# Kernel tuning notes

Measured on AMD Instinct MI355X. Metric: run time of the kernel, lower is better.

Reference implementation:

```python
import jax, jax.numpy as jnp
import numpy as np

HIDDEN = 768

def setup_inputs() -> dict:
    key = jax.random.key(0)
    ks = jax.random.split(key, 7)
    x = jax.random.normal(ks[0], (4, 4096, HIDDEN), dtype=jnp.float32)
    s = 1.0 / np.sqrt(HIDDEN)
    Wq = jax.random.uniform(ks[1], (HIDDEN, HIDDEN), minval=-s, maxval=s, dtype=jnp.float32)
    Wk = jax.random.uniform(ks[2], (HIDDEN, HIDDEN), minval=-s, maxval=s, dtype=jnp.float32)
    Wv = jax.random.uniform(ks[3], (HIDDEN, HIDDEN), minval=-s, maxval=s, dtype=jnp.float32)
    bq = jax.random.uniform(ks[4], (HIDDEN,), minval=-s, maxval=s, dtype=jnp.float32)
    bk = jax.random.uniform(ks[5], (HIDDEN,), minval=-s, maxval=s, dtype=jnp.float32)
    bv = jax.random.uniform(ks[6], (HIDDEN,), minval=-s, maxval=s, dtype=jnp.float32)
    return {"x": x, "Wq": Wq, "bq": bq, "Wk": Wk, "bk": bk, "Wv": Wv, "bv": bv}

def reference(x, Wq, bq, Wk, bk, Wv, bv):
    # q,k,v: [b, s, d]
    q = jnp.einsum('bsd,de->bse', x, Wq.T) + bq
    k = jnp.einsum('bsd,de->bse', x, Wk.T) + bk
    v = jnp.einsum('bsd,de->bse', x, Wv.T) + bv
    scale = 1.0 / jnp.sqrt(jnp.asarray(x.shape[-1], dtype=x.dtype))
    scores = jnp.einsum('bqd,bkd->bqk', q, k) * scale  # [b, s, s]
    attn = jax.nn.softmax(scores, axis=-1)
    return jnp.einsum('bqk,bkd->bqd', attn, v)
```

## Files before the change

kernel.cpp:

```cpp
#include <hip/hip_runtime.h>
#include <stdint.h>

typedef unsigned short u16;
typedef __attribute__((ext_vector_type(8))) short    bf16x8;
typedef __attribute__((ext_vector_type(4))) float    f32x4;

__device__ __forceinline__ u16 f2bf(float f) {
    unsigned u = __float_as_uint(f);
    u = (u + 0x7fffu + ((u >> 16) & 1u)) >> 16;
    return (u16)u;
}

__global__ __launch_bounds__(256) void cast_bf16_kernel(const float* __restrict__ in,
                                                        u16* __restrict__ out, int n4) {
    int i = blockIdx.x * 256 + threadIdx.x;
    if (i < n4) {
        float4 f = ((const float4*)in)[i];
        ushort4 o;
        o.x = f2bf(f.x); o.y = f2bf(f.y); o.z = f2bf(f.z); o.w = f2bf(f.w);
        ((ushort4*)out)[i] = o;
    }
}

__global__ __launch_bounds__(256) void cast3_bf16_kernel(const float* __restrict__ w0,
                                                         const float* __restrict__ w1,
                                                         const float* __restrict__ w2,
                                                         u16* __restrict__ out) {
    const float* src = (blockIdx.y == 0) ? w0 : (blockIdx.y == 1) ? w1 : w2;
    int i = blockIdx.x * 256 + threadIdx.x;
    float4 f = ((const float4*)src)[i];
    ushort4 o;
    o.x = f2bf(f.x); o.y = f2bf(f.y); o.z = f2bf(f.z); o.w = f2bf(f.w);
    ((ushort4*)out)[(size_t)blockIdx.y * 147456 + i] = o;
}

__global__ __launch_bounds__(256) void transpose_bf16_kernel(const u16* __restrict__ V,
                                                             u16* __restrict__ Vt,
                                                             float* __restrict__ rsum) {
    __shared__ u16 tile[32][33];
    const int t = threadIdx.x;
    if (blockIdx.x == 0 && blockIdx.z == 0) {
        int idx = blockIdx.y * 256 + t;
        if (idx < 16384) rsum[idx] = 0.f;
    }
    const size_t z = blockIdx.z;
    const u16* Vb  = V  + z * (size_t)4096 * 2304;
    u16*       Vtb = Vt + z * (size_t)768 * 4096;
    const int c0 = blockIdx.x * 32;
    const int r0 = blockIdx.y * 32;
    const int lr = t >> 3;
    const int lc = (t & 7) * 4;
    ushort4 in = *(const ushort4*)&Vb[(size_t)(r0 + lr) * 2304 + c0 + lc];
    tile[lr][lc + 0] = in.x; tile[lr][lc + 1] = in.y;
    tile[lr][lc + 2] = in.z; tile[lr][lc + 3] = in.w;
    __syncthreads();
    ushort4 o;
    o.x = tile[lc + 0][lr]; o.y = tile[lc + 1][lr];
    o.z = tile[lc + 2][lr]; o.w = tile[lc + 3][lr];
    *(ushort4*)&Vtb[(size_t)(c0 + lr) * 4096 + r0 + lc] = o;
}

template <int EPI, int WN, int NBX, int GRP, int NGRID, int NBY, int MINW>
__global__ __launch_bounds__(256, MINW) void gemm_bt_kernel(
        const u16* __restrict__ A, const u16* __restrict__ B, void* __restrict__ Cv,
        const float* __restrict__ b0, const float* __restrict__ b1, const float* __restrict__ b2,
        float* __restrict__ rs, float s2, int K,
        int lda, int ldb, int ldc, long batchA, long batchB, long batchC) {
    __shared__ __align__(16) u16 As[128 * 64];
    __shared__ __align__(16) u16 Bs[32 * WN * 64];

    constexpr int SPX = NGRID / (8 * NBX);
    const int lin = blockIdx.x;
    const int c = lin & 7, p = lin >> 3;
    const int bxi = p % GRP;
    const int rest = p / GRP;
    const int s = rest % SPX;
    const int g = rest / SPX;
    const int bx = g * GRP + bxi;
    const int strip = c * SPX + s;
    const int by = strip % NBY;
    const int bz = strip / NBY;

    const int t = threadIdx.x;
    const long z = bz;
    const u16* Ab = A + z * batchA + (long)by * 128 * lda;
    const u16* Bb = B + z * batchB + (long)bx * (32 * WN) * ldb;

    const int lane = t & 63;
    const int wave = t >> 6;
    const int wm = wave >> 1, wn = wave & 1;
    const int quad = lane >> 4;
    const int frow = lane & 15;
    const int cc0 = quad ^ (frow & 7);

    f32x4 acc[4][WN];
#pragma unroll
    for (int i = 0; i < 4; i++)
#pragma unroll
        for (int j = 0; j < WN; j++)
#pragma unroll
            for (int e = 0; e < 4; e++) acc[i][j][e] = 0.f;

    int srow[WN], scol[WN];
#pragma unroll
    for (int j = 0; j < WN; j++) {
        const int d = t + j * 256;
        srow[j] = d >> 3;
        scol[j] = ((d & 7) ^ (srow[j] & 7)) * 8;
    }

    bf16x8 ra[4], rb[WN];
#pragma unroll
    for (int j = 0; j < 4; j++)
        ra[j] = *(const bf16x8*)(Ab + (long)srow[j] * lda + scol[j]);
#pragma unroll
    for (int j = 0; j < WN; j++)
        rb[j] = *(const bf16x8*)(Bb + (long)srow[j] * ldb + scol[j]);

    for (int kt = 0; kt < K; kt += 64) {
#pragma unroll
        for (int j = 0; j < 4; j++)
            *(bf16x8*)&As[(t + j * 256) * 8] = ra[j];
#pragma unroll
        for (int j = 0; j < WN; j++)
            *(bf16x8*)&Bs[(t + j * 256) * 8] = rb[j];
        __syncthreads();

        if (kt + 64 < K) {
            const int kn = kt + 64;
#pragma unroll
            for (int j = 0; j < 4; j++)
                ra[j] = *(const bf16x8*)(Ab + (long)srow[j] * lda + kn + scol[j]);
#pragma unroll
            for (int j = 0; j < WN; j++)
                rb[j] = *(const bf16x8*)(Bb + (long)srow[j] * ldb + kn + scol[j]);
        }

#pragma unroll
        for (int kk = 0; kk < 2; kk++) {
            const int cc = (cc0 ^ (kk * 4)) * 8;
            bf16x8 bfr[WN];
#pragma unroll
            for (int j = 0; j < WN; j++)
                bfr[j] = *(const bf16x8*)&Bs[(wn * WN * 16 + j * 16 + frow) * 64 + cc];
#pragma unroll
            for (int i = 0; i < 4; i++) {
                bf16x8 af = *(const bf16x8*)&As[(wm * 64 + i * 16 + frow) * 64 + cc];
#pragma unroll
                for (int j = 0; j < WN; j++)
                    acc[i][j] = __builtin_amdgcn_mfma_f32_16x16x32_bf16(af, bfr[j], acc[i][j], 0, 0, 0);
            }
        }
        __syncthreads();
    }

    const int m_base = by * 128 + wm * 64;
    const int n_base = bx * (32 * WN) + wn * (16 * WN);

    if (EPI == 0) {
        const int seg = n_base / 768;
        const float* bp = (seg == 0) ? b0 : (seg == 1) ? b1 : b2;
        u16* C = (u16*)Cv + z * batchC;
#pragma unroll
        for (int j = 0; j < WN; j++) {
            const int col = n_base + j * 16 + frow;
            const float bb = bp[col - seg * 768];
#pragma unroll
            for (int i = 0; i < 4; i++) {
                const int row0 = m_base + i * 16 + quad * 4;
#pragma unroll
                for (int r = 0; r < 4; r++)
                    C[(long)(row0 + r) * ldc + col] = f2bf(acc[i][j][r] + bb);
            }
        }
    } else if (EPI == 1) {
        u16* C = (u16*)Cv + z * batchC;
        float rowpart[4][4];
#pragma unroll
        for (int i = 0; i < 4; i++)
#pragma unroll
            for (int r = 0; r < 4; r++) rowpart[i][r] = 0.f;
#pragma unroll
        for (int i = 0; i < 4; i++) {
            const int row0 = m_base + i * 16 + quad * 4;
#pragma unroll
            for (int j = 0; j < WN; j++) {
                const int col = n_base + j * 16 + frow;
#pragma unroll
                for (int r = 0; r < 4; r++) {
                    float e = exp2f(acc[i][j][r] * s2);
                    C[(long)(row0 + r) * ldc + col] = f2bf(e);
                    rowpart[i][r] += e;
                }
            }
        }
#pragma unroll
        for (int i = 0; i < 4; i++)
#pragma unroll
            for (int r = 0; r < 4; r++) {
                float v = rowpart[i][r];
                v += __shfl_xor(v, 1); v += __shfl_xor(v, 2);
                v += __shfl_xor(v, 4); v += __shfl_xor(v, 8);
                if (frow == 0)
                    atomicAdd(&rs[z * 4096 + m_base + i * 16 + quad * 4 + r], v);
            }
    } else {
        float* C = (float*)Cv + z * batchC;
#pragma unroll
        for (int i = 0; i < 4; i++) {
            const int row0 = m_base + i * 16 + quad * 4;
            float inv[4];
#pragma unroll
            for (int r = 0; r < 4; r++) inv[r] = 1.0f / rs[z * 4096 + row0 + r];
#pragma unroll
            for (int j = 0; j < WN; j++) {
                const int col = n_base + j * 16 + frow;
#pragma unroll
                for (int r = 0; r < 4; r++)
                    C[(long)(row0 + r) * ldc + col] = acc[i][j][r] * inv[r];
            }
        }
    }
}

extern "C" void kernel_launch(void* const* d_in, const int* in_sizes, int n_in,
                              void* d_out, int out_size, void* d_ws, size_t ws_size,
                              hipStream_t stream) {
    const float* x  = (const float*)d_in[0];
    const float* Wq = (const float*)d_in[1];
    const float* bq = (const float*)d_in[2];
    const float* Wk = (const float*)d_in[3];
    const float* bk = (const float*)d_in[4];
    const float* Wv = (const float*)d_in[5];
    const float* bv = (const float*)d_in[6];
    float* out = (float*)d_out;

    uint8_t* ws = (uint8_t*)d_ws;
    u16*   xb   = (u16*)(ws + 0);
    u16*   Vt   = (u16*)(ws + 0);
    u16*   QKV  = (u16*)(ws + 25165824);
    u16*   E    = (u16*)(ws + 100663296);
    u16*   Wqkv = (u16*)(ws + 234881024);
    float* rsum = (float*)(ws + 234881024);

    cast_bf16_kernel<<<12288, 256, 0, stream>>>(x, xb, 3145728);
    cast3_bf16_kernel<<<dim3(576, 3), 256, 0, stream>>>(Wq, Wk, Wv, Wqkv);

    gemm_bt_kernel<0, 4, 18, 6, 2304, 128, 3><<<2304, 256, 0, stream>>>(
        xb, Wqkv, QKV, bq, bk, bv, nullptr, 0.f, 768, 768, 768, 2304, 0, 0, 0);

    transpose_bf16_kernel<<<dim3(24, 128, 4), 256, 0, stream>>>(QKV + 1536, Vt, rsum);

    gemm_bt_kernel<1, 8, 16, 4, 2048, 32, 2><<<2048, 256, 0, stream>>>(
        QKV, QKV + 768, E, nullptr, nullptr, nullptr, rsum, 0.05205954822032348f,
        768, 2304, 2304, 4096, (long)4096 * 2304, (long)4096 * 2304, (long)4096 * 4096);

    gemm_bt_kernel<2, 4, 6, 6, 768, 32, 3><<<768, 256, 0, stream>>>(
        E, Vt, out, nullptr, nullptr, nullptr, rsum, 0.f,
        4096, 4096, 4096, 768, (long)4096 * 4096, (long)768 * 4096, (long)4096 * 768);
}
```

Measured before the change: 418.7 us.

## Add 8-wave 256x256 GEMM with direct global-to-LDS pipelined loads for attention

Adds a new 512-thread GEMM kernel that works on 256x256 output tiles. It stages K-tiles straight from global memory into LDS with global_load_lds, uses a swizzled LDS layout, and interleaves loads with MFMA sub-phases using barriers, vmcnt waits and setprio. The kernel replaces the previous QK^T exp and PV GEMM launches, with fused epilogues for exp plus row-sum atomics and for normalisation. The aim is higher MFMA utilisation and more data reuse per block. The PV launch now has only 192 blocks on the chip, which risks under-filling the compute units.

```diff
diff --git a/kernel.cpp b/kernel.cpp
--- a/kernel.cpp
+++ b/kernel.cpp
@@ -223,6 +223,177 @@
     }
 }
 
+__device__ __forceinline__ void gload16(const u16* src, u16* dst) {
+    __builtin_amdgcn_global_load_lds((const __attribute__((address_space(1))) void*)src,
+                                     (__attribute__((address_space(3))) void*)dst,
+                                     16, 0, 0);
+}
+
+template <int EPI, int NBX, int NBY, int NT>
+__global__ __launch_bounds__(512, 2) void gemm8_kernel(
+        const u16* __restrict__ A, const u16* __restrict__ B, void* __restrict__ Cv,
+        float* __restrict__ rs, float s2,
+        int lda, int ldb, int ldc, long batchA, long batchB, long batchC) {
+    static_assert(NT >= 3, "pipeline needs >=3 K-tiles");
+    __shared__ __align__(16) u16 lds[2][4][8192];
+
+    constexpr int NWG = NBX * NBY * 4;
+    const int lin = blockIdx.x;
+    const int swz = (lin & 7) * (NWG / 8) + (lin >> 3);
+    const int bz  = swz / (NBX * NBY);
+    const int rr_ = swz % (NBX * NBY);
+    const int by  = rr_ / NBX, bx = rr_ % NBX;
+
+    const int t_   = threadIdx.x;
+    const int lane = t_ & 63;
+    const int wave = t_ >> 6;
+    const int wm = wave >> 2, wn = wave & 3;
+    const int frow = lane & 15, quad = lane >> 4;
+
+    const u16* Ab = A + (long)bz * batchA + (long)by * 256 * lda;
+    const u16* Bb = B + (long)bz * batchB + (long)bx * 256 * ldb;
+
+    const int srow = ((t_ >> 3) << 1) | ((t_ >> 2) & 1);
+    const int scol = ((t_ & 3) ^ ((t_ >> 3) & 3)) * 8;
+    const int dstu = wave * 512;
+
+    const int rdoff = (frow >> 1) * 64
+                    + ((frow & 1) * 4 + (quad ^ ((frow >> 1) & 3))) * 8;
+    const int aoff = wm * 128 * 32 + rdoff;
+    const int boff = wn * 64 * 32 + rdoff;
+
+    f32x4 acc[8][4];
+#pragma unroll
+    for (int i = 0; i < 8; i++)
+#pragma unroll
+        for (int j = 0; j < 4; j++)
+#pragma unroll
+            for (int e = 0; e < 4; e++) acc[i][j][e] = 0.f;
+
+    auto STAGE = [&](int buf, int reg, const u16* gb, int ld_, int kofs) {
+#pragma unroll
+        for (int j = 0; j < 2; ++j) {
+            const u16* sp = gb + (long)(srow + j * 128) * ld_ + kofs + scol;
+            gload16(sp, &lds[buf][reg][dstu + j * 4096]);
+        }
+    };
+
+    STAGE(0, 2, Bb, ldb, 0);
+    STAGE(0, 0, Ab, lda, 0);
+    STAGE(0, 3, Bb, ldb, 32);
+    STAGE(0, 1, Ab, lda, 32);
+    STAGE(1, 2, Bb, ldb, 64);
+    STAGE(1, 0, Ab, lda, 64);
+    STAGE(1, 3, Bb, ldb, 96);
+    asm volatile("s_waitcnt vmcnt(6)" ::: "memory");
+    __builtin_amdgcn_s_barrier();
+
+#define MFMA16(SUB)                                                              \
+    __builtin_amdgcn_s_setprio(1);                                               \
+    _Pragma("unroll")                                                            \
+    for (int i = 0; i < 4; ++i)                                                  \
+        _Pragma("unroll")                                                        \
+        for (int j = 0; j < 4; ++j)                                              \
+            acc[(SUB) * 4 + i][j] = __builtin_amdgcn_mfma_f32_16x16x32_bf16(     \
+                a[i], b[j], acc[(SUB) * 4 + i][j], 0, 0, 0);                     \
+    __builtin_amdgcn_s_setprio(0);
+
+#pragma unroll 2
+    for (int t = 0; t < NT; ++t) {
+        const int cur = t & 1, nxt = cur ^ 1;
+        const u16* A0 = (const u16*)lds[cur][0];
+        const u16* A1 = (const u16*)lds[cur][1];
+        const u16* B0 = (const u16*)lds[cur][2];
+        const u16* B1 = (const u16*)lds[cur][3];
+        bf16x8 a[4], b[4];
+
+#pragma unroll
+        for (int i = 0; i < 4; ++i) a[i] = *(const bf16x8*)&A0[aoff + i * 512];
+#pragma unroll
+        for (int j = 0; j < 4; ++j) b[j] = *(const bf16x8*)&B0[boff + j * 512];
+        if (t + 1 < NT) STAGE(nxt, 1, Ab, lda, (t + 1) * 64 + 32);
+        __builtin_amdgcn_s_barrier();
+        asm volatile("s_waitcnt lgkmcnt(0)" ::: "memory");
+        MFMA16(0)
+        __builtin_amdgcn_s_barrier();
+
+#pragma unroll
+        for (int i = 0; i < 4; ++i) a[i] = *(const bf16x8*)&A0[aoff + 2048 + i * 512];
+        if (t + 2 < NT) STAGE(cur, 2, Bb, ldb, (t + 2) * 64);
+        __builtin_amdgcn_s_barrier();
+        asm volatile("s_waitcnt lgkmcnt(0)" ::: "memory");
+        MFMA16(1)
+        __builtin_amdgcn_s_barrier();
+
+#pragma unroll
+        for (int i = 0; i < 4; ++i) a[i] = *(const bf16x8*)&A1[aoff + i * 512];
+#pragma unroll
+        for (int j = 0; j < 4; ++j) b[j] = *(const bf16x8*)&B1[boff + j * 512];
+        if (t + 2 < NT) STAGE(cur, 0, Ab, lda, (t + 2) * 64);
+        __builtin_amdgcn_s_barrier();
+        asm volatile("s_waitcnt lgkmcnt(0)" ::: "memory");
+        MFMA16(0)
+        __builtin_amdgcn_s_barrier();
+
+#pragma unroll
+        for (int i = 0; i < 4; ++i) a[i] = *(const bf16x8*)&A1[aoff + 2048 + i * 512];
+        if (t + 2 < NT) STAGE(cur, 3, Bb, ldb, (t + 2) * 64 + 32);
+        __builtin_amdgcn_s_barrier();
+        asm volatile("s_waitcnt lgkmcnt(0)" ::: "memory");
+        MFMA16(1)
+        if (t + 2 < NT)      asm volatile("s_waitcnt vmcnt(6)" ::: "memory");
+        else if (t + 1 < NT) asm volatile("s_waitcnt vmcnt(0)" ::: "memory");
+        __builtin_amdgcn_s_barrier();
+    }
+#undef MFMA16
+
+    const int m_base = by * 256 + wm * 128;
+    const int n_base = bx * 256 + wn * 64;
+    const long z = bz;
+
+    if (EPI == 1) {
+        u16* C = (u16*)Cv + z * batchC;
+#pragma unroll
+        for (int ig = 0; ig < 8; ++ig) {
+            const int row0 = m_base + ig * 16 + quad * 4;
+            float rp[4] = {0.f, 0.f, 0.f, 0.f};
+#pragma unroll
+            for (int j = 0; j < 4; ++j) {
+                const int col = n_base + j * 16 + frow;
+#pragma unroll
+                for (int r = 0; r < 4; ++r) {
+                    float e = exp2f(acc[ig][j][r] * s2);
+                    C[(long)(row0 + r) * ldc + col] = f2bf(e);
+                    rp[r] += e;
+                }
+            }
+#pragma unroll
+            for (int r = 0; r < 4; ++r) {
+                float v = rp[r];
+                v += __shfl_xor(v, 1); v += __shfl_xor(v, 2);
+                v += __shfl_xor(v, 4); v += __shfl_xor(v, 8);
+                if (frow == 0) atomicAdd(&rs[z * 4096 + row0 + r], v);
+            }
+        }
+    } else {
+        float* C = (float*)Cv + z * batchC;
+#pragma unroll
+        for (int ig = 0; ig < 8; ++ig) {
+            const int row0 = m_base + ig * 16 + quad * 4;
+            float inv[4];
+#pragma unroll
+            for (int r = 0; r < 4; ++r) inv[r] = 1.0f / rs[z * 4096 + row0 + r];
+#pragma unroll
+            for (int j = 0; j < 4; ++j) {
+                const int col = n_base + j * 16 + frow;
+#pragma unroll
+                for (int r = 0; r < 4; ++r)
+                    C[(long)(row0 + r) * ldc + col] = acc[ig][j][r] * inv[r];
+            }
+        }
+    }
+}
+
 extern "C" void kernel_launch(void* const* d_in, const int* in_sizes, int n_in,
                               void* d_out, int out_size, void* d_ws, size_t ws_size,
                               hipStream_t stream) {
@@ -251,11 +422,11 @@
 
     transpose_bf16_kernel<<<dim3(24, 128, 4), 256, 0, stream>>>(QKV + 1536, Vt, rsum);
 
-    gemm_bt_kernel<1, 8, 16, 4, 2048, 32, 2><<<2048, 256, 0, stream>>>(
-        QKV, QKV + 768, E, nullptr, nullptr, nullptr, rsum, 0.05205954822032348f,
-        768, 2304, 2304, 4096, (long)4096 * 2304, (long)4096 * 2304, (long)4096 * 4096);
-
-    gemm_bt_kernel<2, 4, 6, 6, 768, 32, 3><<<768, 256, 0, stream>>>(
-        E, Vt, out, nullptr, nullptr, nullptr, rsum, 0.f,
-        4096, 4096, 4096, 768, (long)4096 * 4096, (long)768 * 4096, (long)4096 * 768);
-}
+    gemm8_kernel<1, 16, 16, 12><<<1024, 512, 0, stream>>>(
+        QKV, QKV + 768, E, rsum, 0.05205954822032348f,
+        2304, 2304, 4096, (long)4096 * 2304, (long)4096 * 2304, (long)4096 * 4096);
+
+    gemm8_kernel<2, 3, 16, 64><<<192, 512, 0, stream>>>(
+        E, Vt, out, rsum, 0.f,
+        4096, 4096, 768, (long)4096 * 4096, (long)768 * 4096, (long)4096 * 768);
+}
```

Result: slower. 439.0 us (+4.8%).
